# Optimization experiments

Measured on AMD Instinct MI355X. Metric: run time of the kernel, lower is better.

Reference implementation:

```python
import jax, jax.numpy as jnp
import numpy as np

HEADS = 9
MODEL_DIM = 256
LN_EPS = 1e-5


def _relative_features(h, w):
    # grid[i, j] = (i, j); rel[i, j, k, l] = (k - i, l - j)
    r = jnp.arange(h if h >= w else w)
    gi, gj = jnp.meshgrid(jnp.arange(h), jnp.arange(w), indexing='ij')
    grid = jnp.stack([gi, gj], axis=-1).astype(jnp.float32)          # (h, w, 2)
    rel = grid[None, None, :, :, :] - grid[:, :, None, None, :]       # (h, w, h, w, 2)
    cross = (rel[..., 0] * rel[..., 1])[..., None]
    return jnp.concatenate([rel, rel ** 2, cross], axis=-1)           # (h, w, h, w, 5)


def _layer_norm(x, gamma, beta):
    mu = jnp.mean(x, axis=-1, keepdims=True)
    var = jnp.var(x, axis=-1, keepdims=True)
    return (x - mu) * jax.lax.rsqrt(var + LN_EPS) * gamma + beta


def setup_inputs() -> dict:
    key = jax.random.key(0)
    ks = jax.random.split(key, 6)
    bs, h, w = 16, 32, 32
    hidden_state = jax.random.normal(ks[0], (bs, h, w, MODEL_DIM), dtype=jnp.float32)
    attention_centers = 2.0 * jax.random.normal(ks[1], (HEADS, 2), dtype=jnp.float32)
    attention_spreads = jnp.eye(2, dtype=jnp.float32)[None] + 0.01 * jax.random.normal(
        ks[2], (HEADS, 2, 2), dtype=jnp.float32)
    # torch Linear(in=heads*model_dim, out=model_dim): weight (out, in)
    fan_in = HEADS * MODEL_DIM
    bound = 1.0 / np.sqrt(fan_in)
    value_w = jax.random.uniform(ks[3], (MODEL_DIM, fan_in), jnp.float32, -bound, bound)
    value_b = jax.random.uniform(ks[4], (MODEL_DIM,), jnp.float32, -bound, bound)
    ln_gamma = jnp.ones((MODEL_DIM,), jnp.float32)
    ln_beta = jnp.zeros((MODEL_DIM,), jnp.float32)
    return {
        'hidden_state': hidden_state,
        'attention_centers': attention_centers,
        'attention_spreads': attention_spreads,
        'value_w': value_w,
        'value_b': value_b,
        'ln_gamma': ln_gamma,
        'ln_beta': ln_beta,
    }


def reference(hidden_state, attention_centers, attention_spreads, value_w, value_b,
              ln_gamma, ln_beta):
    bs, h, w, d = hidden_state.shape
    # pre_norm=True: normalize first, residual uses normalized hidden (as in source)
    x = _layer_norm(hidden_state, ln_gamma, ln_beta)

    # per-head quadratic target vector u (faithful to source, incl. the (c + mu_2) term)
    inv_cov = jnp.einsum('hij,hkj->hik', attention_spreads, attention_spreads)
    a, b, c = inv_cov[:, 0, 0], inv_cov[:, 0, 1], inv_cov[:, 1, 1]
    mu1, mu2 = attention_centers[:, 0], attention_centers[:, 1]
    u = -0.5 * jnp.stack(
        [-2 * (a * mu1 + b * mu2), -2 * (c + mu2 + b * mu1), a, c, 2 * b], axis=-1)  # (H, 5)

    R = _relative_features(h, w)                                      # (h, w, h, w, 5)
    scores = jnp.einsum('ijkld,hd->ijhkl', R, u)                      # (h, w, H, h, w)
    probs = jax.nn.softmax(scores.reshape(h, w, HEADS, h * w), axis=-1)
    probs = probs.reshape(h, w, HEADS, h, w)
    # dropout prob = 0 (eval mode)

    context = jnp.einsum('ijhkl,bkld->bijhd', probs, x)               # (bs, h, w, H, d)
    context = context.reshape(bs, h, w, HEADS * d)
    output = context @ value_w.T + value_b
    output = output + x
    return output, probs
```

## Files before the change

kernel.cpp:

```cpp
#include <hip/hip_runtime.h>
#include <hip/hip_bf16.h>
#include <stdint.h>

typedef __bf16 bf16;
typedef __bf16 bf16x4 __attribute__((ext_vector_type(4)));
typedef __bf16 bf16x8 __attribute__((ext_vector_type(8)));
typedef float  f32x4  __attribute__((ext_vector_type(4)));

#define GLDS16(g, l) __builtin_amdgcn_global_load_lds(                      \
    (const __attribute__((address_space(1))) void*)(g),                     \
    (__attribute__((address_space(3))) void*)(l), 16, 0, 0)

#define BARX() do { __builtin_amdgcn_s_barrier();                            \
                    __builtin_amdgcn_sched_barrier(0); } while (0)
#define VMW(n) do { asm volatile("s_waitcnt vmcnt(" #n ")" ::: "memory");    \
                    __builtin_amdgcn_sched_barrier(0); } while (0)

__global__ __launch_bounds__(256) void k_ln(const float* __restrict__ hs,
                                            const float* __restrict__ gamma,
                                            const float* __restrict__ beta,
                                            bf16* __restrict__ xb) {
  int wid = threadIdx.x >> 6, lane = threadIdx.x & 63;
  size_t row = (size_t)blockIdx.x * 4 + wid;
  const float4* p = (const float4*)(hs + row * 256);
  float4 v = p[lane];
  float s  = v.x + v.y + v.z + v.w;
  float s2 = v.x*v.x + v.y*v.y + v.z*v.z + v.w*v.w;
#pragma unroll
  for (int o = 32; o; o >>= 1) { s += __shfl_xor(s, o); s2 += __shfl_xor(s2, o); }
  float mu  = s * (1.0f/256.0f);
  float var = s2 * (1.0f/256.0f) - mu*mu;
  float rs  = rsqrtf(var + 1e-5f);
  float4 g = ((const float4*)gamma)[lane];
  float4 b = ((const float4*)beta)[lane];
  bf16x4 o4;
  o4[0] = (bf16)((v.x - mu) * rs * g.x + b.x);
  o4[1] = (bf16)((v.y - mu) * rs * g.y + b.y);
  o4[2] = (bf16)((v.z - mu) * rs * g.z + b.z);
  o4[3] = (bf16)((v.w - mu) * rs * g.w + b.w);
  *(bf16x4*)(xb + row * 256 + lane * 4) = o4;
}

__global__ __launch_bounds__(256) void k_xt(const bf16* __restrict__ xb,
                                            bf16* __restrict__ xt) {
  __shared__ bf16 tile[64][65];
  int kl0 = blockIdx.x * 64, d0 = blockIdx.y * 64, b = blockIdx.z;
  int t = threadIdx.x;
  int r = t >> 2, c0 = (t & 3) * 16;
  const bf16* src = xb + ((size_t)(b * 1024 + kl0 + r)) * 256 + d0 + c0;
  bf16x8 v0 = *(const bf16x8*)src;
  bf16x8 v1 = *(const bf16x8*)(src + 8);
#pragma unroll
  for (int i = 0; i < 8; i++) { tile[r][c0 + i] = v0[i]; tile[r][c0 + 8 + i] = v1[i]; }
  __syncthreads();
  int dr = t >> 2, k0 = (t & 3) * 16;
  bf16x8 w0, w1;
#pragma unroll
  for (int i = 0; i < 8; i++) { w0[i] = tile[k0 + i][dr]; w1[i] = tile[k0 + 8 + i][dr]; }
  bf16* dst = xt + ((size_t)(b * 256 + d0 + dr)) * 1024 + kl0 + k0;
  *(bf16x8*)dst = w0;
  *(bf16x8*)(dst + 8) = w1;
}

__global__ __launch_bounds__(256) void k_vwb(const float* __restrict__ vw,
                                             bf16* __restrict__ vwb) {
  int i = (blockIdx.x * 256 + threadIdx.x) * 8;
  float4 q0 = *(const float4*)(vw + i);
  float4 q1 = *(const float4*)(vw + i + 4);
  bf16x8 o;
  o[0]=(bf16)q0.x; o[1]=(bf16)q0.y; o[2]=(bf16)q0.z; o[3]=(bf16)q0.w;
  o[4]=(bf16)q1.x; o[5]=(bf16)q1.y; o[6]=(bf16)q1.z; o[7]=(bf16)q1.w;
  *(bf16x8*)(vwb + i) = o;
}

__global__ __launch_bounds__(256) void k_probs(const float* __restrict__ centers,
                                               const float* __restrict__ spreads,
                                               float* __restrict__ pf,
                                               bf16* __restrict__ pb) {
  int bid = blockIdx.x;
  int h  = bid % 9;
  int ij = bid / 9;
  int i = ij >> 5, j = ij & 31;
  float S00 = spreads[h*4+0], S01 = spreads[h*4+1];
  float S10 = spreads[h*4+2], S11 = spreads[h*4+3];
  float a  = S00*S00 + S01*S01;
  float bq = S00*S10 + S01*S11;
  float c  = S10*S10 + S11*S11;
  float mu1 = centers[h*2+0], mu2 = centers[h*2+1];
  float u0 = a*mu1 + bq*mu2;
  float u1 = c + mu2 + bq*mu1;
  float u2 = -0.5f*a, u3 = -0.5f*c, u4 = -bq;
  int t = threadIdx.x;
  float sc[4]; float mx = -1e30f;
#pragma unroll
  for (int s = 0; s < 4; s++) {
    int kl = t*4 + s;
    float d0 = (float)((kl >> 5) - i);
    float d1 = (float)((kl & 31) - j);
    float v = d0*(u0 + u2*d0) + d1*(u1 + u3*d1) + u4*d0*d1;
    sc[s] = v; mx = fmaxf(mx, v);
  }
  __shared__ float red[8];
#pragma unroll
  for (int o = 32; o; o >>= 1) mx = fmaxf(mx, __shfl_xor(mx, o));
  int lane = t & 63, wid = t >> 6;
  if (lane == 0) red[wid] = mx;
  __syncthreads();
  mx = fmaxf(fmaxf(red[0], red[1]), fmaxf(red[2], red[3]));
  float sum = 0.f;
#pragma unroll
  for (int s = 0; s < 4; s++) { sc[s] = __expf(sc[s] - mx); sum += sc[s]; }
#pragma unroll
  for (int o = 32; o; o >>= 1) sum += __shfl_xor(sum, o);
  if (lane == 0) red[4 + wid] = sum;
  __syncthreads();
  sum = red[4] + red[5] + red[6] + red[7];
  float inv = 1.0f / sum;
  float4 o;
  o.x = sc[0]*inv; o.y = sc[1]*inv; o.z = sc[2]*inv; o.w = sc[3]*inv;
  *(float4*)(pf + (size_t)bid*1024 + t*4) = o;
  bf16x4 ob;
  ob[0] = (bf16)o.x; ob[1] = (bf16)o.y; ob[2] = (bf16)o.z; ob[3] = (bf16)o.w;
  *(bf16x4*)(pb + (size_t)bid*1024 + t*4) = ob;
}

__global__ __launch_bounds__(128) void k_sort(const float* __restrict__ centers,
                                              const float* __restrict__ spreads,
                                              int* __restrict__ sorted) {
  __shared__ int nt[72];
  int t = threadIdx.x;
  if (t < 72) {
    int h = t >> 3, mb = t & 7;
    float S00 = spreads[h*4+0], S01 = spreads[h*4+1];
    float S10 = spreads[h*4+2], S11 = spreads[h*4+3];
    float a_ = S00*S00 + S01*S01;
    float b_ = S00*S10 + S01*S11;
    float c_ = S10*S10 + S11*S11;
    float mu1 = centers[h*2+0], mu2 = centers[h*2+1];
    float det = fmaxf(a_*c_ - b_*b_, 1e-6f);
    float A_ = a_*mu1 + b_*mu2;
    float B_ = c_ + mu2 + b_*mu1;
    float ustar = (c_*A_ - b_*B_) / det;
    float lam = fmaxf(a_ - b_*b_/c_, 1e-3f);
    float M_ = __fsqrt_rn(28.0f / lam) + 1.5f;
    float lo_f = (float)(mb*4) + ustar, hi_f = lo_f + 3.0f;
    int k_lo = (int)floorf(fminf(lo_f, 31.0f) - M_);
    int k_hi = (int)ceilf(fmaxf(hi_f, 0.0f) + M_) + 1;
    if (k_lo < 0) k_lo = 0;
    if (k_hi > 32) k_hi = 32;
    if (k_hi <= k_lo) { k_lo = 0; k_hi = 32; }
    nt[t] = k_hi - k_lo;
  }
  __syncthreads();
  if (t < 72) {
    int my = nt[t], r = 0;
#pragma unroll 1
    for (int j = 0; j < 72; j++) {
      int v = nt[j];
      if (v > my || (v == my && j < t)) r++;
    }
    sorted[r] = t;
  }
}

__device__ __forceinline__ bf16x8 frag_ld(const bf16* base, int row, int g) {
  return *(const bf16x8*)(base + row*32 + ((g ^ ((row >> 1) & 3)) << 3));
}

__global__ __launch_bounds__(256, 2) void k_ctx(const bf16* __restrict__ pb,
                                                const bf16* __restrict__ xt,
                                                const float* __restrict__ centers,
                                                const float* __restrict__ spreads,
                                                const int* __restrict__ sorted,
                                                bf16* __restrict__ ctx,
                                                int b0, int nbt) {
  __shared__ bf16 As[3*4096];
  __shared__ bf16 Bs[3*8192];
  int r_  = blockIdx.x / nbt;
  int nb  = blockIdx.x % nbt;
  int cls = sorted[r_];
  int h   = cls >> 3;
  int mb  = cls & 7;
  int ij0 = mb * 128;
  int nrow0 = (b0 + nb) * 256;

  int t = threadIdx.x, lane = t & 63, w = t >> 6;
  int wr = w >> 1, wc = w & 1;
  int g = lane >> 4, rl = lane & 15;

  float S00 = spreads[h*4+0], S01 = spreads[h*4+1];
  float S10 = spreads[h*4+2], S11 = spreads[h*4+3];
  float a_ = S00*S00 + S01*S01;
  float b_ = S00*S10 + S01*S11;
  float c_ = S10*S10 + S11*S11;
  float mu1 = centers[h*2+0], mu2 = centers[h*2+1];
  float det = fmaxf(a_*c_ - b_*b_, 1e-6f);
  float A_ = a_*mu1 + b_*mu2;
  float B_ = c_ + mu2 + b_*mu1;
  float ustar = (c_*A_ - b_*B_) / det;
  float lam = fmaxf(a_ - b_*b_/c_, 1e-3f);
  float M_ = __fsqrt_rn(28.0f / lam) + 1.5f;
  float lo_f = (float)(mb*4) + ustar, hi_f = lo_f + 3.0f;
  int k_lo = (int)floorf(fminf(lo_f, 31.0f) - M_);
  int k_hi = (int)ceilf(fmaxf(hi_f, 0.0f) + M_) + 1;
  if (k_lo < 0) k_lo = 0;
  if (k_hi > 32) k_hi = 32;
  if (k_hi <= k_lo) { k_lo = 0; k_hi = 32; }
  const int NT = k_hi - k_lo;

  f32x4 acc[4][8];
#pragma unroll
  for (int x_ = 0; x_ < 4; x_++)
#pragma unroll
    for (int y_ = 0; y_ < 8; y_++) acc[x_][y_] = (f32x4){0.f,0.f,0.f,0.f};

  int arow = t >> 2;
  int acs  = (t & 3) ^ ((t >> 3) & 3);
  const bf16* a1 = pb + (size_t)(ij0 + arow) * 9216 + h * 1024 + k_lo*32 + acs * 8;
  const bf16* a2 = a1 + (size_t)64 * 9216;
  const bf16* b1 = xt + (size_t)(nrow0 + arow) * 1024 + k_lo*32 + acs * 8;

#define STG(sb, kt) do {                                                    \
    GLDS16(a1 + (kt)*32, ((char*)As) + (sb)*8192 + t*16);                   \
    GLDS16(a2 + (kt)*32, ((char*)As) + (sb)*8192 + 4096 + t*16);            \
    _Pragma("unroll")                                                       \
    for (int q = 0; q < 4; q++)                                             \
      GLDS16(b1 + (size_t)q*64*1024 + (kt)*32,                              \
             ((char*)Bs) + (sb)*16384 + q*4096 + t*16);                     \
  } while (0)

  STG(0, 0);
  if (NT > 1) { STG(1, 1); VMW(6); } else { VMW(0); }
  BARX();

  int cur = 0;
  for (int kt = 0; kt < NT; ++kt) {
    int sb = cur + 2; if (sb >= 3) sb -= 3;
    bf16x8 af[4], bf_[8];
#pragma unroll
    for (int fr = 0; fr < 4; fr++) af[fr]  = frag_ld(As + cur*4096, wr*64 + fr*16 + rl, g);
#pragma unroll
    for (int fn = 0; fn < 8; fn++) bf_[fn] = frag_ld(Bs + cur*8192, wc*128 + fn*16 + rl, g);
    if (kt + 2 < NT) STG(sb, kt + 2);
#pragma unroll
    for (int fr = 0; fr < 4; fr++)
#pragma unroll
      for (int fn = 0; fn < 8; fn++)
        acc[fr][fn] = __builtin_amdgcn_mfma_f32_16x16x32_bf16(af[fr], bf_[fn], acc[fr][fn], 0, 0, 0);
    if (kt + 2 < NT)      VMW(6);
    else if (kt + 1 < NT) VMW(0);
    BARX();
    cur = cur + 1; if (cur >= 3) cur = 0;
  }
#undef STG

#pragma unroll
  for (int fr = 0; fr < 4; fr++) {
    int row = ij0 + wr*64 + fr*16 + g*4;
#pragma unroll
    for (int fn = 0; fn < 8; fn++) {
      int d = wc*128 + fn*16 + rl;
      size_t base = ((size_t)nb*1024 + row) * 2304 + h*256 + d;
      f32x4 a4 = acc[fr][fn];
#pragma unroll
      for (int r = 0; r < 4; r++)
        ctx[base + (size_t)r*2304] = (bf16)a4[r];
    }
  }
}

__global__ __launch_bounds__(512, 1) void k_out(const bf16* __restrict__ ctx,
                                                const bf16* __restrict__ vwb,
                                                const bf16* __restrict__ xb,
                                                const float* __restrict__ vbias,
                                                float* __restrict__ out, int b0) {
  __shared__ bf16 lds[3 * 20480];
  int t = threadIdx.x, lane = t & 63, w = t >> 6;
  int wr = w >> 2, wc = w & 3;
  int g = lane >> 4, rl = lane & 15;
  int r0 = blockIdx.x * 64;
  char* ldsb = (char*)lds;

  f32x4 acc[2][4];
#pragma unroll
  for (int x_ = 0; x_ < 2; x_++)
#pragma unroll
    for (int y_ = 0; y_ < 4; y_++) acc[x_][y_] = (f32x4){0.f,0.f,0.f,0.f};

  int rr  = t >> 3;
  int csw = (t & 7) ^ (rr & 7);
  const bf16* aS = ctx + (size_t)(r0 + rr) * 2304 + csw * 8;
  const bf16* bS = vwb + (size_t)rr * 2304 + csw * 8;

#define STGO(sb, kt) do {                                                     \
    GLDS16(aS + (kt)*64, ldsb + (sb)*40960 + t*16);                           \
    _Pragma("unroll")                                                         \
    for (int q = 0; q < 4; q++)                                               \
      GLDS16(bS + (size_t)q*64*2304 + (kt)*64,                                \
             ldsb + (sb)*40960 + 8192 + q*8192 + t*16);                       \
  } while (0)

  STGO(0, 0); STGO(1, 1);
  VMW(5);
  BARX();

  int cur = 0;
  for (int kt = 0; kt < 36; ++kt) {
    int sb = cur + 2; if (sb >= 3) sb -= 3;
    const char* ab = ldsb + cur*40960;
    const char* bb = ab + 8192;
    bf16x8 af0[2], af1[2], bf0[4], bf1[4];
#pragma unroll
    for (int fr = 0; fr < 2; fr++) {
      int row_ = wr*32 + fr*16 + rl;
      af0[fr] = *(const bf16x8*)(ab + row_*128 + (((g  ) ^ (row_&7)) << 4));
      af1[fr] = *(const bf16x8*)(ab + row_*128 + (((g+4) ^ (row_&7)) << 4));
    }
#pragma unroll
    for (int fn = 0; fn < 4; fn++) {
      int row_ = wc*64 + fn*16 + rl;
      bf0[fn] = *(const bf16x8*)(bb + row_*128 + (((g  ) ^ (row_&7)) << 4));
      bf1[fn] = *(const bf16x8*)(bb + row_*128 + (((g+4) ^ (row_&7)) << 4));
    }
    if (kt + 2 < 36) STGO(sb, kt + 2);
    BARX();
    __builtin_amdgcn_s_setprio(1);
#pragma unroll
    for (int fr = 0; fr < 2; fr++)
#pragma unroll
      for (int fn = 0; fn < 4; fn++) {
        acc[fr][fn] = __builtin_amdgcn_mfma_f32_16x16x32_bf16(af0[fr], bf0[fn], acc[fr][fn], 0, 0, 0);
        acc[fr][fn] = __builtin_amdgcn_mfma_f32_16x16x32_bf16(af1[fr], bf1[fn], acc[fr][fn], 0, 0, 0);
      }
    __builtin_amdgcn_s_setprio(0);
    if (kt + 2 < 36)      VMW(5);
    else if (kt + 1 < 36) VMW(0);
    BARX();
    cur = cur + 1; if (cur >= 3) cur = 0;
  }
#undef STGO

#pragma unroll
  for (int fr = 0; fr < 2; fr++) {
    int rowl = r0 + wr*32 + fr*16 + g*4;
    size_t rowg = (size_t)b0*1024 + rowl;
#pragma unroll
    for (int fn = 0; fn < 4; fn++) {
      int m = wc*64 + fn*16 + rl;
      float bv = vbias[m];
      size_t base = rowg*256 + m;
#pragma unroll
      for (int r = 0; r < 4; r++)
        out[base + (size_t)r*256] = acc[fr][fn][r] + bv + (float)xb[base + (size_t)r*256];
    }
  }
}

extern "C" void kernel_launch(void* const* d_in, const int* in_sizes, int n_in,
                              void* d_out, int out_size, void* d_ws, size_t ws_size,
                              hipStream_t stream) {
  const float* hs      = (const float*)d_in[0];
  const float* centers = (const float*)d_in[1];
  const float* spreads = (const float*)d_in[2];
  const float* vw      = (const float*)d_in[3];
  const float* vb      = (const float*)d_in[4];
  const float* gamma   = (const float*)d_in[5];
  const float* beta    = (const float*)d_in[6];
  float* out     = (float*)d_out;
  float* probs_f = out + 4194304;

  char* ws = (char*)d_ws;
  bf16* xb  = (bf16*)ws;
  bf16* pb  = (bf16*)(ws + 8388608);
  bf16* xt  = (bf16*)(ws + 27262976);
  bf16* vwb = (bf16*)(ws + 35651584);
  bf16* ctx = (bf16*)(ws + 36831232);

  int CB = 16;
  while (CB > 1 && 36831232ull + (size_t)CB * 4718592ull + 512ull > ws_size) CB >>= 1;
  int* sortedp = (int*)(ws + 36831232 + (size_t)CB * 4718592ull);

  k_ln<<<4096, 256, 0, stream>>>(hs, gamma, beta, xb);
  k_xt<<<dim3(16, 4, 16), 256, 0, stream>>>(xb, xt);
  k_probs<<<9216, 256, 0, stream>>>(centers, spreads, probs_f, pb);
  k_vwb<<<288, 256, 0, stream>>>(vw, vwb);
  k_sort<<<1, 128, 0, stream>>>(centers, spreads, sortedp);
  for (int b0 = 0; b0 < 16; b0 += CB) {
    int c = (16 - b0) < CB ? (16 - b0) : CB;
    k_ctx<<<dim3(72 * c), 256, 0, stream>>>(pb, xt, centers, spreads, sortedp, ctx, b0, c);
    k_out<<<dim3(c*16), 512, 0, stream>>>(ctx, vwb, xb, vb, out, b0);
  }
}
```

Baseline: 117.7 us.

## Pre-tile probs and x into MFMA fragment layout, load fragments directly from global

The bf16 probs and transposed activations are now written in a k-tiled layout (32-wide k chunks contiguous per row), so each MFMA fragment is a contiguous 16-byte global load. The context kernel drops its LDS triple-buffered global_load_lds pipeline and barriers, loading fragments straight into registers with register double buffering. This removes LDS traffic and synchronisation, but each wave now loads its own A/B fragments from global or L2 with no cross-wave sharing through LDS, and the strided bf16x4 probs writes may coalesce less well.

```diff
diff --git a/kernel.cpp b/kernel.cpp
--- a/kernel.cpp
+++ b/kernel.cpp
@@ -42,7 +42,7 @@
 }
 
 __global__ __launch_bounds__(256) void k_xt(const bf16* __restrict__ xb,
-                                            bf16* __restrict__ xt) {
+                                            bf16* __restrict__ xt3) {
   __shared__ bf16 tile[64][65];
   int kl0 = blockIdx.x * 64, d0 = blockIdx.y * 64, b = blockIdx.z;
   int t = threadIdx.x;
@@ -57,7 +57,8 @@
   bf16x8 w0, w1;
 #pragma unroll
   for (int i = 0; i < 8; i++) { w0[i] = tile[k0 + i][dr]; w1[i] = tile[k0 + 8 + i][dr]; }
-  bf16* dst = xt + ((size_t)(b * 256 + d0 + dr)) * 1024 + kl0 + k0;
+  int kk = kl0 + k0;
+  bf16* dst = xt3 + ((size_t)(b * 32 + (kk >> 5)) * 256 + d0 + dr) * 32 + (kk & 31);
   *(bf16x8*)dst = w0;
   *(bf16x8*)(dst + 8) = w1;
 }
@@ -76,7 +77,7 @@
 __global__ __launch_bounds__(256) void k_probs(const float* __restrict__ centers,
                                                const float* __restrict__ spreads,
                                                float* __restrict__ pf,
-                                               bf16* __restrict__ pb) {
+                                               bf16* __restrict__ pb2) {
   int bid = blockIdx.x;
   int h  = bid % 9;
   int ij = bid / 9;
@@ -121,7 +122,7 @@
   *(float4*)(pf + (size_t)bid*1024 + t*4) = o;
   bf16x4 ob;
   ob[0] = (bf16)o.x; ob[1] = (bf16)o.y; ob[2] = (bf16)o.z; ob[3] = (bf16)o.w;
-  *(bf16x4*)(pb + (size_t)bid*1024 + t*4) = ob;
+  *(bf16x4*)(pb2 + ((size_t)(h*32 + (t >> 3))*1024 + ij)*32 + (t & 7)*4) = ob;
 }
 
 __global__ __launch_bounds__(128) void k_sort(const float* __restrict__ centers,
@@ -163,26 +164,19 @@
   }
 }
 
-__device__ __forceinline__ bf16x8 frag_ld(const bf16* base, int row, int g) {
-  return *(const bf16x8*)(base + row*32 + ((g ^ ((row >> 1) & 3)) << 3));
-}
-
-__global__ __launch_bounds__(256, 2) void k_ctx(const bf16* __restrict__ pb,
-                                                const bf16* __restrict__ xt,
+__global__ __launch_bounds__(256, 2) void k_ctx(const bf16* __restrict__ pb2,
+                                                const bf16* __restrict__ xt3,
                                                 const float* __restrict__ centers,
                                                 const float* __restrict__ spreads,
                                                 const int* __restrict__ sorted,
                                                 bf16* __restrict__ ctx,
                                                 int b0, int nbt) {
-  __shared__ bf16 As[3*4096];
-  __shared__ bf16 Bs[3*8192];
   int r_  = blockIdx.x / nbt;
   int nb  = blockIdx.x % nbt;
   int cls = sorted[r_];
   int h   = cls >> 3;
   int mb  = cls & 7;
   int ij0 = mb * 128;
-  int nrow0 = (b0 + nb) * 256;
 
   int t = threadIdx.x, lane = t & 63, w = t >> 6;
   int wr = w >> 1, wc = w & 1;
@@ -214,45 +208,45 @@
 #pragma unroll
     for (int y_ = 0; y_ < 8; y_++) acc[x_][y_] = (f32x4){0.f,0.f,0.f,0.f};
 
-  int arow = t >> 2;
-  int acs  = (t & 3) ^ ((t >> 3) & 3);
-  const bf16* a1 = pb + (size_t)(ij0 + arow) * 9216 + h * 1024 + k_lo*32 + acs * 8;
-  const bf16* a2 = a1 + (size_t)64 * 9216;
-  const bf16* b1 = xt + (size_t)(nrow0 + arow) * 1024 + k_lo*32 + acs * 8;
-
-#define STG(sb, kt) do {                                                    \
-    GLDS16(a1 + (kt)*32, ((char*)As) + (sb)*8192 + t*16);                   \
-    GLDS16(a2 + (kt)*32, ((char*)As) + (sb)*8192 + 4096 + t*16);            \
+  const bf16* aP  = pb2 + ((size_t)(h*32 + k_lo)*1024 + ij0 + wr*64 + rl)*32 + g*8;
+  const bf16* bP0 = xt3 + ((size_t)((b0 + nb)*32 + k_lo)*256 + wc*128 + rl)*32 + g*8;
+  const bf16* bP4 = bP0 + 64*32;
+
+#define LOADF(AF, BF, kt) do {                                              \
+    const bf16* a_p  = aP  + (size_t)(kt)*32768;                            \
+    const bf16* b_p  = bP0 + (size_t)(kt)*8192;                             \
+    const bf16* b_p4 = bP4 + (size_t)(kt)*8192;                             \
     _Pragma("unroll")                                                       \
-    for (int q = 0; q < 4; q++)                                             \
-      GLDS16(b1 + (size_t)q*64*1024 + (kt)*32,                              \
-             ((char*)Bs) + (sb)*16384 + q*4096 + t*16);                     \
+    for (int fr = 0; fr < 4; fr++) AF[fr] = *(const bf16x8*)(a_p + fr*512); \
+    _Pragma("unroll")                                                       \
+    for (int fn = 0; fn < 4; fn++) {                                        \
+      BF[fn]   = *(const bf16x8*)(b_p  + fn*512);                           \
+      BF[fn+4] = *(const bf16x8*)(b_p4 + fn*512);                           \
+    }                                                                       \
   } while (0)
 
-  STG(0, 0);
-  if (NT > 1) { STG(1, 1); VMW(6); } else { VMW(0); }
-  BARX();
-
-  int cur = 0;
-  for (int kt = 0; kt < NT; ++kt) {
-    int sb = cur + 2; if (sb >= 3) sb -= 3;
-    bf16x8 af[4], bf_[8];
-#pragma unroll
-    for (int fr = 0; fr < 4; fr++) af[fr]  = frag_ld(As + cur*4096, wr*64 + fr*16 + rl, g);
-#pragma unroll
-    for (int fn = 0; fn < 8; fn++) bf_[fn] = frag_ld(Bs + cur*8192, wc*128 + fn*16 + rl, g);
-    if (kt + 2 < NT) STG(sb, kt + 2);
-#pragma unroll
-    for (int fr = 0; fr < 4; fr++)
-#pragma unroll
-      for (int fn = 0; fn < 8; fn++)
-        acc[fr][fn] = __builtin_amdgcn_mfma_f32_16x16x32_bf16(af[fr], bf_[fn], acc[fr][fn], 0, 0, 0);
-    if (kt + 2 < NT)      VMW(6);
-    else if (kt + 1 < NT) VMW(0);
-    BARX();
-    cur = cur + 1; if (cur >= 3) cur = 0;
-  }
-#undef STG
+#define MFM(AF, BF) do {                                                    \
+    _Pragma("unroll")                                                       \
+    for (int fr = 0; fr < 4; fr++)                                          \
+      _Pragma("unroll")                                                     \
+      for (int fn = 0; fn < 8; fn++)                                        \
+        acc[fr][fn] = __builtin_amdgcn_mfma_f32_16x16x32_bf16(              \
+            AF[fr], BF[fn], acc[fr][fn], 0, 0, 0);                          \
+  } while (0)
+
+  bf16x8 afA[4], bfA[8], afB[4], bfB[8];
+  LOADF(afA, bfA, 0);
+  int kt = 0;
+  while (true) {
+    if (kt + 1 < NT) LOADF(afB, bfB, kt + 1);
+    MFM(afA, bfA);
+    if (++kt >= NT) break;
+    if (kt + 1 < NT) LOADF(afA, bfA, kt + 1);
+    MFM(afB, bfB);
+    if (++kt >= NT) break;
+  }
+#undef LOADF
+#undef MFM
 
 #pragma unroll
   for (int fr = 0; fr < 4; fr++) {
@@ -371,8 +365,8 @@
 
   char* ws = (char*)d_ws;
   bf16* xb  = (bf16*)ws;
-  bf16* pb  = (bf16*)(ws + 8388608);
-  bf16* xt  = (bf16*)(ws + 27262976);
+  bf16* pb2 = (bf16*)(ws + 8388608);
+  bf16* xt3 = (bf16*)(ws + 27262976);
   bf16* vwb = (bf16*)(ws + 35651584);
   bf16* ctx = (bf16*)(ws + 36831232);
 
@@ -381,13 +375,13 @@
   int* sortedp = (int*)(ws + 36831232 + (size_t)CB * 4718592ull);
 
   k_ln<<<4096, 256, 0, stream>>>(hs, gamma, beta, xb);
-  k_xt<<<dim3(16, 4, 16), 256, 0, stream>>>(xb, xt);
-  k_probs<<<9216, 256, 0, stream>>>(centers, spreads, probs_f, pb);
+  k_xt<<<dim3(16, 4, 16), 256, 0, stream>>>(xb, xt3);
+  k_probs<<<9216, 256, 0, stream>>>(centers, spreads, probs_f, pb2);
   k_vwb<<<288, 256, 0, stream>>>(vw, vwb);
   k_sort<<<1, 128, 0, stream>>>(centers, spreads, sortedp);
   for (int b0 = 0; b0 < 16; b0 += CB) {
     int c = (16 - b0) < CB ? (16 - b0) : CB;
-    k_ctx<<<dim3(72 * c), 256, 0, stream>>>(pb, xt, centers, spreads, sortedp, ctx, b0, c);
+    k_ctx<<<dim3(72 * c), 256, 0, stream>>>(pb2, xt3, centers, spreads, sortedp, ctx, b0, c);
     k_out<<<dim3(c*16), 512, 0, stream>>>(ctx, vwb, xb, vb, out, b0);
   }
 }
```

Measured after the change: 447.4 us. 280% more time.

## Store bf16 probs in MFMA fragment layout and load A directly to registers

Applied to the files above, without the earlier changes.

k_probs now writes the bf16 probability copy in a layout arranged by head, key-row tile and query position, so k_ctx can fetch its A-operand fragments straight from global memory into registers. A register double-buffer replaces the LDS staging of A. This removes A's LDS traffic and shrinks shared memory per block, which may raise occupancy, at the cost of scattered 8-byte stores in k_probs and exposed global-load latency in the loop. The sort kernel is also folded into an extra block of k_vwb to save one launch.

```diff
diff --git a/kernel.cpp b/kernel.cpp
--- a/kernel.cpp
+++ b/kernel.cpp
@@ -63,8 +63,48 @@
 }
 
 __global__ __launch_bounds__(256) void k_vwb(const float* __restrict__ vw,
-                                             bf16* __restrict__ vwb) {
-  int i = (blockIdx.x * 256 + threadIdx.x) * 8;
+                                             bf16* __restrict__ vwb,
+                                             const float* __restrict__ centers,
+                                             const float* __restrict__ spreads,
+                                             int* __restrict__ sorted) {
+  __shared__ int nt[72];
+  int t = threadIdx.x;
+  if (blockIdx.x == 288) {
+    if (t < 72) {
+      int h = t >> 3, mb = t & 7;
+      float S00 = spreads[h*4+0], S01 = spreads[h*4+1];
+      float S10 = spreads[h*4+2], S11 = spreads[h*4+3];
+      float a_ = S00*S00 + S01*S01;
+      float b_ = S00*S10 + S01*S11;
+      float c_ = S10*S10 + S11*S11;
+      float mu1 = centers[h*2+0], mu2 = centers[h*2+1];
+      float det = fmaxf(a_*c_ - b_*b_, 1e-6f);
+      float A_ = a_*mu1 + b_*mu2;
+      float B_ = c_ + mu2 + b_*mu1;
+      float ustar = (c_*A_ - b_*B_) / det;
+      float lam = fmaxf(a_ - b_*b_/c_, 1e-3f);
+      float M_ = __fsqrt_rn(28.0f / lam) + 1.5f;
+      float lo_f = (float)(mb*4) + ustar, hi_f = lo_f + 3.0f;
+      int k_lo = (int)floorf(fminf(lo_f, 31.0f) - M_);
+      int k_hi = (int)ceilf(fmaxf(hi_f, 0.0f) + M_) + 1;
+      if (k_lo < 0) k_lo = 0;
+      if (k_hi > 32) k_hi = 32;
+      if (k_hi <= k_lo) { k_lo = 0; k_hi = 32; }
+      nt[t] = k_hi - k_lo;
+    }
+    __syncthreads();
+    if (t < 72) {
+      int my = nt[t], r = 0;
+#pragma unroll 1
+      for (int j = 0; j < 72; j++) {
+        int v = nt[j];
+        if (v > my || (v == my && j < t)) r++;
+      }
+      sorted[r] = t;
+    }
+    return;
+  }
+  int i = (blockIdx.x * 256 + t) * 8;
   float4 q0 = *(const float4*)(vw + i);
   float4 q1 = *(const float4*)(vw + i + 4);
   bf16x8 o;
@@ -76,7 +116,7 @@
 __global__ __launch_bounds__(256) void k_probs(const float* __restrict__ centers,
                                                const float* __restrict__ spreads,
                                                float* __restrict__ pf,
-                                               bf16* __restrict__ pb) {
+                                               bf16* __restrict__ pb2) {
   int bid = blockIdx.x;
   int h  = bid % 9;
   int ij = bid / 9;
@@ -121,60 +161,20 @@
   *(float4*)(pf + (size_t)bid*1024 + t*4) = o;
   bf16x4 ob;
   ob[0] = (bf16)o.x; ob[1] = (bf16)o.y; ob[2] = (bf16)o.z; ob[3] = (bf16)o.w;
-  *(bf16x4*)(pb + (size_t)bid*1024 + t*4) = ob;
-}
-
-__global__ __launch_bounds__(128) void k_sort(const float* __restrict__ centers,
-                                              const float* __restrict__ spreads,
-                                              int* __restrict__ sorted) {
-  __shared__ int nt[72];
-  int t = threadIdx.x;
-  if (t < 72) {
-    int h = t >> 3, mb = t & 7;
-    float S00 = spreads[h*4+0], S01 = spreads[h*4+1];
-    float S10 = spreads[h*4+2], S11 = spreads[h*4+3];
-    float a_ = S00*S00 + S01*S01;
-    float b_ = S00*S10 + S01*S11;
-    float c_ = S10*S10 + S11*S11;
-    float mu1 = centers[h*2+0], mu2 = centers[h*2+1];
-    float det = fmaxf(a_*c_ - b_*b_, 1e-6f);
-    float A_ = a_*mu1 + b_*mu2;
-    float B_ = c_ + mu2 + b_*mu1;
-    float ustar = (c_*A_ - b_*B_) / det;
-    float lam = fmaxf(a_ - b_*b_/c_, 1e-3f);
-    float M_ = __fsqrt_rn(28.0f / lam) + 1.5f;
-    float lo_f = (float)(mb*4) + ustar, hi_f = lo_f + 3.0f;
-    int k_lo = (int)floorf(fminf(lo_f, 31.0f) - M_);
-    int k_hi = (int)ceilf(fmaxf(hi_f, 0.0f) + M_) + 1;
-    if (k_lo < 0) k_lo = 0;
-    if (k_hi > 32) k_hi = 32;
-    if (k_hi <= k_lo) { k_lo = 0; k_hi = 32; }
-    nt[t] = k_hi - k_lo;
-  }
-  __syncthreads();
-  if (t < 72) {
-    int my = nt[t], r = 0;
-#pragma unroll 1
-    for (int j = 0; j < 72; j++) {
-      int v = nt[j];
-      if (v > my || (v == my && j < t)) r++;
-    }
-    sorted[r] = t;
-  }
+  *(bf16x4*)(pb2 + ((size_t)(h*32 + (t >> 3))*1024 + ij)*32 + (t & 7)*4) = ob;
 }
 
 __device__ __forceinline__ bf16x8 frag_ld(const bf16* base, int row, int g) {
   return *(const bf16x8*)(base + row*32 + ((g ^ ((row >> 1) & 3)) << 3));
 }
 
-__global__ __launch_bounds__(256, 2) void k_ctx(const bf16* __restrict__ pb,
+__global__ __launch_bounds__(256, 2) void k_ctx(const bf16* __restrict__ pb2,
                                                 const bf16* __restrict__ xt,
                                                 const float* __restrict__ centers,
                                                 const float* __restrict__ spreads,
                                                 const int* __restrict__ sorted,
                                                 bf16* __restrict__ ctx,
                                                 int b0, int nbt) {
-  __shared__ bf16 As[3*4096];
   __shared__ bf16 Bs[3*8192];
   int r_  = blockIdx.x / nbt;
   int nb  = blockIdx.x % nbt;
@@ -216,43 +216,76 @@
 
   int arow = t >> 2;
   int acs  = (t & 3) ^ ((t >> 3) & 3);
-  const bf16* a1 = pb + (size_t)(ij0 + arow) * 9216 + h * 1024 + k_lo*32 + acs * 8;
-  const bf16* a2 = a1 + (size_t)64 * 9216;
   const bf16* b1 = xt + (size_t)(nrow0 + arow) * 1024 + k_lo*32 + acs * 8;
+  const bf16* aP = pb2 + ((size_t)(h*32 + k_lo)*1024 + ij0 + wr*64 + rl)*32 + g*8;
 
 #define STG(sb, kt) do {                                                    \
-    GLDS16(a1 + (kt)*32, ((char*)As) + (sb)*8192 + t*16);                   \
-    GLDS16(a2 + (kt)*32, ((char*)As) + (sb)*8192 + 4096 + t*16);            \
     _Pragma("unroll")                                                       \
     for (int q = 0; q < 4; q++)                                             \
       GLDS16(b1 + (size_t)q*64*1024 + (kt)*32,                              \
              ((char*)Bs) + (sb)*16384 + q*4096 + t*16);                     \
   } while (0)
 
+#define LOADA(AF, kt) do {                                                  \
+    const bf16* a_p = aP + (size_t)(kt)*32768;                              \
+    _Pragma("unroll")                                                       \
+    for (int fr = 0; fr < 4; fr++)                                          \
+      AF[fr] = *(const bf16x8*)(a_p + fr*512);                              \
+  } while (0)
+
+#define MFM(AF, BF) do {                                                    \
+    _Pragma("unroll")                                                       \
+    for (int fr = 0; fr < 4; fr++)                                          \
+      _Pragma("unroll")                                                     \
+      for (int fn = 0; fn < 8; fn++)                                        \
+        acc[fr][fn] = __builtin_amdgcn_mfma_f32_16x16x32_bf16(              \
+            AF[fr], BF[fn], acc[fr][fn], 0, 0, 0);                          \
+  } while (0)
+
+  bf16x8 afA[4], afB[4];
   STG(0, 0);
-  if (NT > 1) { STG(1, 1); VMW(6); } else { VMW(0); }
+  if (NT > 1) STG(1, 1);
+  __builtin_amdgcn_sched_barrier(0);
+  LOADA(afA, 0);
+  if (NT > 1) VMW(8); else VMW(4);
   BARX();
 
-  int cur = 0;
-  for (int kt = 0; kt < NT; ++kt) {
-    int sb = cur + 2; if (sb >= 3) sb -= 3;
-    bf16x8 af[4], bf_[8];
-#pragma unroll
-    for (int fr = 0; fr < 4; fr++) af[fr]  = frag_ld(As + cur*4096, wr*64 + fr*16 + rl, g);
-#pragma unroll
-    for (int fn = 0; fn < 8; fn++) bf_[fn] = frag_ld(Bs + cur*8192, wc*128 + fn*16 + rl, g);
-    if (kt + 2 < NT) STG(sb, kt + 2);
-#pragma unroll
-    for (int fr = 0; fr < 4; fr++)
-#pragma unroll
-      for (int fn = 0; fn < 8; fn++)
-        acc[fr][fn] = __builtin_amdgcn_mfma_f32_16x16x32_bf16(af[fr], bf_[fn], acc[fr][fn], 0, 0, 0);
-    if (kt + 2 < NT)      VMW(6);
-    else if (kt + 1 < NT) VMW(0);
-    BARX();
-    cur = cur + 1; if (cur >= 3) cur = 0;
+  int cur = 0, kt = 0;
+  while (true) {
+    {
+      bf16x8 bf_[8];
+#pragma unroll
+      for (int fn = 0; fn < 8; fn++) bf_[fn] = frag_ld(Bs + cur*8192, wc*128 + fn*16 + rl, g);
+      int sb = cur + 2; if (sb >= 3) sb -= 3;
+      if (kt + 2 < NT) STG(sb, kt + 2);
+      __builtin_amdgcn_sched_barrier(0);
+      if (kt + 1 < NT) LOADA(afB, kt + 1);
+      MFM(afA, bf_);
+      if (kt + 1 >= NT) break;
+      if (kt + 2 < NT) VMW(8); else VMW(4);
+      BARX();
+      cur = cur + 1; if (cur >= 3) cur = 0;
+      kt++;
+    }
+    {
+      bf16x8 bf_[8];
+#pragma unroll
+      for (int fn = 0; fn < 8; fn++) bf_[fn] = frag_ld(Bs + cur*8192, wc*128 + fn*16 + rl, g);
+      int sb = cur + 2; if (sb >= 3) sb -= 3;
+      if (kt + 2 < NT) STG(sb, kt + 2);
+      __builtin_amdgcn_sched_barrier(0);
+      if (kt + 1 < NT) LOADA(afA, kt + 1);
+      MFM(afB, bf_);
+      if (kt + 1 >= NT) break;
+      if (kt + 2 < NT) VMW(8); else VMW(4);
+      BARX();
+      cur = cur + 1; if (cur >= 3) cur = 0;
+      kt++;
+    }
   }
 #undef STG
+#undef LOADA
+#undef MFM
 
 #pragma unroll
   for (int fr = 0; fr < 4; fr++) {
@@ -371,7 +404,7 @@
 
   char* ws = (char*)d_ws;
   bf16* xb  = (bf16*)ws;
-  bf16* pb  = (bf16*)(ws + 8388608);
+  bf16* pb2 = (bf16*)(ws + 8388608);
   bf16* xt  = (bf16*)(ws + 27262976);
   bf16* vwb = (bf16*)(ws + 35651584);
   bf16* ctx = (bf16*)(ws + 36831232);
@@ -382,12 +415,11 @@
 
   k_ln<<<4096, 256, 0, stream>>>(hs, gamma, beta, xb);
   k_xt<<<dim3(16, 4, 16), 256, 0, stream>>>(xb, xt);
-  k_probs<<<9216, 256, 0, stream>>>(centers, spreads, probs_f, pb);
-  k_vwb<<<288, 256, 0, stream>>>(vw, vwb);
-  k_sort<<<1, 128, 0, stream>>>(centers, spreads, sortedp);
+  k_probs<<<9216, 256, 0, stream>>>(centers, spreads, probs_f, pb2);
+  k_vwb<<<289, 256, 0, stream>>>(vw, vwb, centers, spreads, sortedp);
   for (int b0 = 0; b0 < 16; b0 += CB) {
     int c = (16 - b0) < CB ? (16 - b0) : CB;
-    k_ctx<<<dim3(72 * c), 256, 0, stream>>>(pb, xt, centers, spreads, sortedp, ctx, b0, c);
+    k_ctx<<<dim3(72 * c), 256, 0, stream>>>(pb2, xt, centers, spreads, sortedp, ctx, b0, c);
     k_out<<<dim3(c*16), 512, 0, stream>>>(ctx, vwb, xb, vb, out, b0);
   }
 }
```

Measured after the change: 113.5 us. 3.5% less time.
